# Optimization experiments

Measured on AMD Instinct MI355X. Metric: run time of the kernel, lower is better.

## Reference

```python
import jax, jax.numpy as jnp
import numpy as np

N = 8192
MARGIN = 0.2
LAMB = 0.012
ITERS = 5


def setup_inputs() -> dict:
    key = jax.random.key(0)
    # sims in [0,1): cosine-similarity-like scores; exp(-(1-s)/lamb) needs s near [0,1]
    sims = jax.random.uniform(key, (N, N), dtype=jnp.float32)
    return {"sims": sims}


def _ot(sims):
    # Sinkhorn-Knopp normalization, r = c = ones so (r/u) == 1/u, (c/v) == 1/v
    P = jnp.exp(-(1.0 - sims) / LAMB)
    P = P / jnp.sum(P)  # global normalization (dims [-2,-1])
    for _ in range(ITERS):
        u = P.sum(axis=-1, keepdims=True)   # row sums  [N,1]
        P = P / u
        v = P.sum(axis=-2, keepdims=True)   # col sums  [1,N]
        P = P / v
    return P


def reference(sims):
    P = _ot(sims)
    d = jnp.diagonal(P)                     # [N]
    eye = jnp.eye(P.shape[0], dtype=bool)
    # cost_im: anchor = column diagonal (d[j]); cost_s: anchor = row diagonal (d[i])
    cost_im = jnp.where(eye, 0.0, jnp.maximum(P - d[None, :] + MARGIN, 0.0))
    cost_s = jnp.where(eye, 0.0, jnp.maximum(P - d[:, None] + MARGIN, 0.0))
    # max_violation = False -> sum over all hinge terms
    return cost_s.sum() + cost_im.sum()
```

## Files before the change

### kernel.cpp

```cpp
#include <hip/hip_runtime.h>


#define NN 8192u
#define MARGIN 0.2f
#define KF (1.4426950408889634f / 0.012f)

__device__ __forceinline__ float fexp2(float x) { return __builtin_amdgcn_exp2f(x); }
__device__ __forceinline__ float frcp(float x) { return __builtin_amdgcn_rcpf(x); }

__device__ __forceinline__ void unpk4(uint q, float& f0, float& f1, float& f2,
                                      float& f3) {
  auto lo = __builtin_amdgcn_cvt_pk_f32_fp8((int)q, false);
  auto hi = __builtin_amdgcn_cvt_pk_f32_fp8((int)q, true);
  f0 = lo[0]; f1 = lo[1]; f2 = hi[0]; f3 = hi[1];
}

__device__ __forceinline__ float blk_reduce(float v, float* red) {
#pragma unroll
  for (int off = 32; off; off >>= 1) v += __shfl_down(v, off, 64);
  const int lane = threadIdx.x & 63, wid = threadIdx.x >> 6;
  __syncthreads();
  if (lane == 0) red[wid] = v;
  __syncthreads();
  return red[0] + red[1] + red[2] + red[3];
}

__global__ __launch_bounds__(256) void k_pass0(const float* __restrict__ sims,
                                               uint* __restrict__ Qw,
                                               float* __restrict__ R,
                                               float* __restrict__ Qd,
                                               float* __restrict__ Cs0,
                                               float* __restrict__ out) {
  __shared__ float red[4];
  const uint row = blockIdx.x;
  const uint t = threadIdx.x;
  float acc = 0.f;
#pragma unroll
  for (uint ch = 0; ch < 8; ++ch) {
    const uint col = ch * 1024u + t * 4u;
    const float4 s = *(const float4*)(sims + (size_t)row * NN + col);
    const float p0 = fexp2((s.x - 1.f) * KF);
    const float p1 = fexp2((s.y - 1.f) * KF);
    const float p2 = fexp2((s.z - 1.f) * KF);
    const float p3 = fexp2((s.w - 1.f) * KF);
    int pk = 0;
    pk = __builtin_amdgcn_cvt_pk_fp8_f32(p0, p1, pk, false);
    pk = __builtin_amdgcn_cvt_pk_fp8_f32(p2, p3, pk, true);
    Qw[((size_t)row * NN + col) >> 2] = (uint)pk;
    float q0, q1, q2, q3;
    unpk4((uint)pk, q0, q1, q2, q3);
    acc += (q0 + q1) + (q2 + q3);
    if (col == (row & ~3u)) {
      const uint sel = row & 3u;
      Qd[row] = sel == 0u ? q0 : sel == 1u ? q1 : sel == 2u ? q2 : q3;
    }
  }
  const float s = blk_reduce(acc, red);
  if (t == 0) R[row] = frcp(s);
  if (row < 32u) Cs0[row * 256u + t] = 0.f;
  if (row == 0 && t == 0) *out = 0.f;
}

__global__ __launch_bounds__(256) void k_colmv(const uint* __restrict__ Qw,
                                               const float* __restrict__ R,
                                               float* __restrict__ dst,
                                               float* __restrict__ zero_other) {
  const uint t = threadIdx.x;
  const uint col = blockIdx.x * 1024u + t * 4u;
  const uint row0 = blockIdx.y * 128u;
  if (blockIdx.y == 0u) {
    float4 z; z.x = z.y = z.z = z.w = 0.f;
    *(float4*)(zero_other + col) = z;
  }
  float a0 = 0.f, a1 = 0.f, a2 = 0.f, a3 = 0.f;
  const uint* qp = Qw + (((size_t)row0 * NN + col) >> 2);
#pragma unroll 4
  for (uint rr = 0; rr < 128u; ++rr) {
    const float Rr = R[row0 + rr];
    float f0, f1, f2, f3;
    unpk4(qp[rr * 2048u], f0, f1, f2, f3);
    a0 = fmaf(f0, Rr, a0);
    a1 = fmaf(f1, Rr, a1);
    a2 = fmaf(f2, Rr, a2);
    a3 = fmaf(f3, Rr, a3);
  }
  atomicAdd(dst + col + 0, a0);
  atomicAdd(dst + col + 1, a1);
  atomicAdd(dst + col + 2, a2);
  atomicAdd(dst + col + 3, a3);
}

__global__ __launch_bounds__(256) void k_rowmv(const uint* __restrict__ Qw,
                                               const float* __restrict__ Csrc,
                                               float* __restrict__ R) {
  __shared__ float ldsC[NN];
  __shared__ float red[4];
  const uint t = threadIdx.x;
  for (uint c = t * 4u; c < NN; c += 1024u) {
    const float4 s = *(const float4*)(Csrc + c);
    float4 o;
    o.x = frcp(s.x); o.y = frcp(s.y); o.z = frcp(s.z); o.w = frcp(s.w);
    *(float4*)(ldsC + c) = o;
  }
  __syncthreads();
#pragma unroll
  for (uint r = 0; r < 8u; ++r) {
    const uint row = blockIdx.x * 8u + r;
    float acc = 0.f;
#pragma unroll
    for (uint ch = 0; ch < 2u; ++ch) {
      const uint col = ch * 4096u + t * 16u;
      const float4 c0 = *(const float4*)(ldsC + col);
      const float4 c1 = *(const float4*)(ldsC + col + 4);
      const float4 c2 = *(const float4*)(ldsC + col + 8);
      const float4 c3 = *(const float4*)(ldsC + col + 12);
      const uint4 q = *(const uint4*)(Qw + (size_t)row * 2048u + (col >> 2));
      float a0, a1, a2, a3, b0, b1, b2, b3;
      unpk4(q.x, a0, a1, a2, a3);
      unpk4(q.y, b0, b1, b2, b3);
      acc += a0 * c0.x + a1 * c0.y + a2 * c0.z + a3 * c0.w;
      acc += b0 * c1.x + b1 * c1.y + b2 * c1.z + b3 * c1.w;
      unpk4(q.z, a0, a1, a2, a3);
      unpk4(q.w, b0, b1, b2, b3);
      acc += a0 * c2.x + a1 * c2.y + a2 * c2.z + a3 * c2.w;
      acc += b0 * c3.x + b1 * c3.y + b2 * c3.z + b3 * c3.w;
    }
    const float s = blk_reduce(acc, red);
    if (t == 0) R[row] = frcp(s);
  }
}

__global__ __launch_bounds__(256) void k_loss(const uint* __restrict__ Qw,
                                              const float* __restrict__ R,
                                              const float* __restrict__ Cs,
                                              const float* __restrict__ Qd,
                                              float* __restrict__ out) {
  __shared__ float red[4];
  const uint t = threadIdx.x;
  const uint col = blockIdx.x * 1024u + t * 4u;
  const uint row0 = blockIdx.y * 128u;
  const float4 cs4 = *(const float4*)(Cs + col);
  const float4 r4 = *(const float4*)(R + col);
  const float4 qd4 = *(const float4*)(Qd + col);
  const float ci0 = frcp(cs4.x), ci1 = frcp(cs4.y), ci2 = frcp(cs4.z),
              ci3 = frcp(cs4.w);
  const float d0 = qd4.x * r4.x * ci0;
  const float d1 = qd4.y * r4.y * ci1;
  const float d2 = qd4.z * r4.z * ci2;
  const float d3 = qd4.w * r4.w * ci3;
  float acc = 0.f;
  const uint* qp = Qw + (((size_t)row0 * NN + col) >> 2);
  for (uint rr = 0; rr < 128u; ++rr) {
    const uint row = row0 + rr;
    const float Rr = R[row];
    const float dr = Qd[row] * Rr * frcp(Cs[row]);
    float f0, f1, f2, f3;
    unpk4(qp[rr * 2048u], f0, f1, f2, f3);
    float p, h;
    p = f0 * Rr * ci0;
    h = fmaxf(p - d0 + MARGIN, 0.f) + fmaxf(p - dr + MARGIN, 0.f);
    acc += (row == col + 0u) ? 0.f : h;
    p = f1 * Rr * ci1;
    h = fmaxf(p - d1 + MARGIN, 0.f) + fmaxf(p - dr + MARGIN, 0.f);
    acc += (row == col + 1u) ? 0.f : h;
    p = f2 * Rr * ci2;
    h = fmaxf(p - d2 + MARGIN, 0.f) + fmaxf(p - dr + MARGIN, 0.f);
    acc += (row == col + 2u) ? 0.f : h;
    p = f3 * Rr * ci3;
    h = fmaxf(p - d3 + MARGIN, 0.f) + fmaxf(p - dr + MARGIN, 0.f);
    acc += (row == col + 3u) ? 0.f : h;
  }
  const float s = blk_reduce(acc, red);
  if (t == 0) atomicAdd(out, s);
}

extern "C" void kernel_launch(void* const* d_in, const int* in_sizes, int n_in,
                              void* d_out, int out_size, void* d_ws,
                              size_t ws_size, hipStream_t stream) {
  const float* sims = (const float*)d_in[0];
  float* out = (float*)d_out;
  uint* Qw = (uint*)d_ws;
  float* fb = (float*)((char*)d_ws + (size_t)NN * NN);
  float* R = fb;
  float* Cs[2] = {fb + NN, fb + 2 * NN};
  float* Qd = fb + 3 * NN;

  k_pass0<<<8192, 256, 0, stream>>>(sims, Qw, R, Qd, Cs[0], out);
  for (int k = 0; k < 5; ++k) {
    k_colmv<<<dim3(8, 64), 256, 0, stream>>>(Qw, R, Cs[k & 1], Cs[(k + 1) & 1]);
    if (k < 4) k_rowmv<<<1024, 256, 0, stream>>>(Qw, Cs[k & 1], R);
  }
  k_loss<<<dim3(8, 64), 256, 0, stream>>>(Qw, R, Cs[0], Qd, out);
}
```

Baseline: 563.7 us.

## Fuse all Sinkhorn passes into one persistent kernel with grid barriers

Replaces the sequence of separate exp, column-sum, row-sum and loss kernels with a single persistent kernel of 256 blocks of 1024 threads that synchronize through a global atomic barrier. Each block owns 32 rows, so its row-sum and loss work reuses the same slice of the fp8 matrix. Column sums are built from per-block partials written to a workspace buffer, then reduced and added atomically. This removes launch gaps and changes the cache access pattern. In exchange it depends on all blocks being co-resident and on a ready-flag and counter protocol whose reset across launches may race.

```diff
diff --git a/kernel.cpp b/kernel.cpp
--- a/kernel.cpp
+++ b/kernel.cpp
@@ -4,174 +4,188 @@
 #define NN 8192u
 #define MARGIN 0.2f
 #define KF (1.4426950408889634f / 0.012f)
+#define NBLK 256u
+#define NTHR 1024u
 
 __device__ __forceinline__ float fexp2(float x) { return __builtin_amdgcn_exp2f(x); }
 __device__ __forceinline__ float frcp(float x) { return __builtin_amdgcn_rcpf(x); }
 
-__device__ __forceinline__ void unpk4(uint q, float& f0, float& f1, float& f2,
-                                      float& f3) {
-  auto lo = __builtin_amdgcn_cvt_pk_f32_fp8((int)q, false);
-  auto hi = __builtin_amdgcn_cvt_pk_f32_fp8((int)q, true);
-  f0 = lo[0]; f1 = lo[1]; f2 = hi[0]; f3 = hi[1];
-}
-
-__device__ __forceinline__ float blk_reduce(float v, float* red) {
-#pragma unroll
-  for (int off = 32; off; off >>= 1) v += __shfl_down(v, off, 64);
-  const int lane = threadIdx.x & 63, wid = threadIdx.x >> 6;
+__device__ __forceinline__ void unpk8(uint2 q, float* f) {
+  auto a = __builtin_amdgcn_cvt_pk_f32_fp8((int)q.x, false);
+  auto b = __builtin_amdgcn_cvt_pk_f32_fp8((int)q.x, true);
+  auto c = __builtin_amdgcn_cvt_pk_f32_fp8((int)q.y, false);
+  auto d = __builtin_amdgcn_cvt_pk_f32_fp8((int)q.y, true);
+  f[0] = a[0]; f[1] = a[1]; f[2] = b[0]; f[3] = b[1];
+  f[4] = c[0]; f[5] = c[1]; f[6] = d[0]; f[7] = d[1];
+}
+
+__device__ __forceinline__ void gbarrier(uint* bar, uint n, uint tid) {
   __syncthreads();
-  if (lane == 0) red[wid] = v;
+  if (tid == 0) {
+    __threadfence();
+    atomicAdd(bar, 1u);
+    const uint tgt = NBLK * n;
+    while (atomicAdd(bar, 0u) < tgt) __builtin_amdgcn_s_sleep(8);
+    __threadfence();
+  }
   __syncthreads();
-  return red[0] + red[1] + red[2] + red[3];
-}
-
-__global__ __launch_bounds__(256) void k_pass0(const float* __restrict__ sims,
-                                               uint* __restrict__ Qw,
-                                               float* __restrict__ R,
-                                               float* __restrict__ Qd,
-                                               float* __restrict__ Cs0,
-                                               float* __restrict__ out) {
-  __shared__ float red[4];
-  const uint row = blockIdx.x;
-  const uint t = threadIdx.x;
-  float acc = 0.f;
-#pragma unroll
-  for (uint ch = 0; ch < 8; ++ch) {
-    const uint col = ch * 1024u + t * 4u;
-    const float4 s = *(const float4*)(sims + (size_t)row * NN + col);
-    const float p0 = fexp2((s.x - 1.f) * KF);
-    const float p1 = fexp2((s.y - 1.f) * KF);
-    const float p2 = fexp2((s.z - 1.f) * KF);
-    const float p3 = fexp2((s.w - 1.f) * KF);
-    int pk = 0;
-    pk = __builtin_amdgcn_cvt_pk_fp8_f32(p0, p1, pk, false);
-    pk = __builtin_amdgcn_cvt_pk_fp8_f32(p2, p3, pk, true);
-    Qw[((size_t)row * NN + col) >> 2] = (uint)pk;
-    float q0, q1, q2, q3;
-    unpk4((uint)pk, q0, q1, q2, q3);
-    acc += (q0 + q1) + (q2 + q3);
-    if (col == (row & ~3u)) {
-      const uint sel = row & 3u;
-      Qd[row] = sel == 0u ? q0 : sel == 1u ? q1 : sel == 2u ? q2 : q3;
-    }
-  }
-  const float s = blk_reduce(acc, red);
-  if (t == 0) R[row] = frcp(s);
-  if (row < 32u) Cs0[row * 256u + t] = 0.f;
-  if (row == 0 && t == 0) *out = 0.f;
-}
-
-__global__ __launch_bounds__(256) void k_colmv(const uint* __restrict__ Qw,
-                                               const float* __restrict__ R,
-                                               float* __restrict__ dst,
-                                               float* __restrict__ zero_other) {
-  const uint t = threadIdx.x;
-  const uint col = blockIdx.x * 1024u + t * 4u;
-  const uint row0 = blockIdx.y * 128u;
-  if (blockIdx.y == 0u) {
-    float4 z; z.x = z.y = z.z = z.w = 0.f;
-    *(float4*)(zero_other + col) = z;
-  }
-  float a0 = 0.f, a1 = 0.f, a2 = 0.f, a3 = 0.f;
-  const uint* qp = Qw + (((size_t)row0 * NN + col) >> 2);
-#pragma unroll 4
-  for (uint rr = 0; rr < 128u; ++rr) {
-    const float Rr = R[row0 + rr];
-    float f0, f1, f2, f3;
-    unpk4(qp[rr * 2048u], f0, f1, f2, f3);
-    a0 = fmaf(f0, Rr, a0);
-    a1 = fmaf(f1, Rr, a1);
-    a2 = fmaf(f2, Rr, a2);
-    a3 = fmaf(f3, Rr, a3);
-  }
-  atomicAdd(dst + col + 0, a0);
-  atomicAdd(dst + col + 1, a1);
-  atomicAdd(dst + col + 2, a2);
-  atomicAdd(dst + col + 3, a3);
-}
-
-__global__ __launch_bounds__(256) void k_rowmv(const uint* __restrict__ Qw,
-                                               const float* __restrict__ Csrc,
-                                               float* __restrict__ R) {
-  __shared__ float ldsC[NN];
-  __shared__ float red[4];
-  const uint t = threadIdx.x;
-  for (uint c = t * 4u; c < NN; c += 1024u) {
-    const float4 s = *(const float4*)(Csrc + c);
-    float4 o;
-    o.x = frcp(s.x); o.y = frcp(s.y); o.z = frcp(s.z); o.w = frcp(s.w);
-    *(float4*)(ldsC + c) = o;
+}
+
+__global__ __launch_bounds__(NTHR) void k_fused(
+    const float* __restrict__ sims, uint* __restrict__ Qw,
+    float* __restrict__ part, float* __restrict__ R, float* __restrict__ CsA,
+    float* __restrict__ CsB, float* __restrict__ Qd, uint* __restrict__ ctl,
+    float* __restrict__ out) {
+  const uint b = blockIdx.x, tid = threadIdx.x;
+  const uint w = tid >> 6, lane = tid & 63u;
+  __shared__ float red[512];
+  uint* ready = ctl;
+  uint* bar = ctl + 1;
+
+  if (b == 0 && tid == 0) {
+    atomicExch(bar, 0u);
+    __threadfence();
+    atomicExch(ready, 0xC0FFEEu);
+  }
+  if (b != 0 && tid == 0) {
+    while (atomicAdd(ready, 0u) != 0xC0FFEEu) __builtin_amdgcn_s_sleep(8);
+    __threadfence();
   }
   __syncthreads();
-#pragma unroll
-  for (uint r = 0; r < 8u; ++r) {
-    const uint row = blockIdx.x * 8u + r;
+  uint bn = 0;
+
+#pragma unroll
+  for (uint q = 0; q < 2u; ++q) {
+    const uint row = b * 32u + q * 16u + w;
+    const uint dit = row >> 8, dl = (row >> 2) & 63u, sel = row & 3u;
     float acc = 0.f;
-#pragma unroll
-    for (uint ch = 0; ch < 2u; ++ch) {
-      const uint col = ch * 4096u + t * 16u;
-      const float4 c0 = *(const float4*)(ldsC + col);
-      const float4 c1 = *(const float4*)(ldsC + col + 4);
-      const float4 c2 = *(const float4*)(ldsC + col + 8);
-      const float4 c3 = *(const float4*)(ldsC + col + 12);
-      const uint4 q = *(const uint4*)(Qw + (size_t)row * 2048u + (col >> 2));
-      float a0, a1, a2, a3, b0, b1, b2, b3;
-      unpk4(q.x, a0, a1, a2, a3);
-      unpk4(q.y, b0, b1, b2, b3);
-      acc += a0 * c0.x + a1 * c0.y + a2 * c0.z + a3 * c0.w;
-      acc += b0 * c1.x + b1 * c1.y + b2 * c1.z + b3 * c1.w;
-      unpk4(q.z, a0, a1, a2, a3);
-      unpk4(q.w, b0, b1, b2, b3);
-      acc += a0 * c2.x + a1 * c2.y + a2 * c2.z + a3 * c2.w;
-      acc += b0 * c3.x + b1 * c3.y + b2 * c3.z + b3 * c3.w;
-    }
-    const float s = blk_reduce(acc, red);
-    if (t == 0) R[row] = frcp(s);
-  }
-}
-
-__global__ __launch_bounds__(256) void k_loss(const uint* __restrict__ Qw,
-                                              const float* __restrict__ R,
-                                              const float* __restrict__ Cs,
-                                              const float* __restrict__ Qd,
-                                              float* __restrict__ out) {
-  __shared__ float red[4];
-  const uint t = threadIdx.x;
-  const uint col = blockIdx.x * 1024u + t * 4u;
-  const uint row0 = blockIdx.y * 128u;
-  const float4 cs4 = *(const float4*)(Cs + col);
-  const float4 r4 = *(const float4*)(R + col);
-  const float4 qd4 = *(const float4*)(Qd + col);
-  const float ci0 = frcp(cs4.x), ci1 = frcp(cs4.y), ci2 = frcp(cs4.z),
-              ci3 = frcp(cs4.w);
-  const float d0 = qd4.x * r4.x * ci0;
-  const float d1 = qd4.y * r4.y * ci1;
-  const float d2 = qd4.z * r4.z * ci2;
-  const float d3 = qd4.w * r4.w * ci3;
-  float acc = 0.f;
-  const uint* qp = Qw + (((size_t)row0 * NN + col) >> 2);
-  for (uint rr = 0; rr < 128u; ++rr) {
-    const uint row = row0 + rr;
-    const float Rr = R[row];
-    const float dr = Qd[row] * Rr * frcp(Cs[row]);
-    float f0, f1, f2, f3;
-    unpk4(qp[rr * 2048u], f0, f1, f2, f3);
-    float p, h;
-    p = f0 * Rr * ci0;
-    h = fmaxf(p - d0 + MARGIN, 0.f) + fmaxf(p - dr + MARGIN, 0.f);
-    acc += (row == col + 0u) ? 0.f : h;
-    p = f1 * Rr * ci1;
-    h = fmaxf(p - d1 + MARGIN, 0.f) + fmaxf(p - dr + MARGIN, 0.f);
-    acc += (row == col + 1u) ? 0.f : h;
-    p = f2 * Rr * ci2;
-    h = fmaxf(p - d2 + MARGIN, 0.f) + fmaxf(p - dr + MARGIN, 0.f);
-    acc += (row == col + 2u) ? 0.f : h;
-    p = f3 * Rr * ci3;
-    h = fmaxf(p - d3 + MARGIN, 0.f) + fmaxf(p - dr + MARGIN, 0.f);
-    acc += (row == col + 3u) ? 0.f : h;
-  }
-  const float s = blk_reduce(acc, red);
-  if (t == 0) atomicAdd(out, s);
+    for (uint it = 0; it < 32u; ++it) {
+      const uint col = it * 256u + lane * 4u;
+      const float4 s = *(const float4*)(sims + (size_t)row * NN + col);
+      const float p0 = fexp2((s.x - 1.f) * KF);
+      const float p1 = fexp2((s.y - 1.f) * KF);
+      const float p2 = fexp2((s.z - 1.f) * KF);
+      const float p3 = fexp2((s.w - 1.f) * KF);
+      int pk = 0;
+      pk = __builtin_amdgcn_cvt_pk_fp8_f32(p0, p1, pk, false);
+      pk = __builtin_amdgcn_cvt_pk_fp8_f32(p2, p3, pk, true);
+      Qw[((size_t)row * NN + col) >> 2] = (uint)pk;
+      auto lo = __builtin_amdgcn_cvt_pk_f32_fp8(pk, false);
+      auto hi = __builtin_amdgcn_cvt_pk_f32_fp8(pk, true);
+      acc += (lo[0] + lo[1]) + (hi[0] + hi[1]);
+      if (it == dit && lane == dl)
+        Qd[row] = sel == 0u ? lo[0] : sel == 1u ? lo[1] : sel == 2u ? hi[0] : hi[1];
+    }
+#pragma unroll
+    for (int o = 32; o; o >>= 1) acc += __shfl_down(acc, o, 64);
+    if (lane == 0) R[row] = frcp(acc);
+  }
+  if (tid < 32u) CsA[b * 32u + tid] = 0.f;
+  if (b == 0 && tid == 0) *out = 0.f;
+
+  for (uint k = 0; k < 5u; ++k) {
+    float* dst = (k & 1u) ? CsB : CsA;
+    float* oth = (k & 1u) ? CsA : CsB;
+    gbarrier(bar, ++bn, tid);
+    {
+      const uint j0 = tid * 8u;
+      float a[8];
+#pragma unroll
+      for (int i = 0; i < 8; ++i) a[i] = 0.f;
+      for (uint r = 0; r < 32u; ++r) {
+        const uint row = b * 32u + r;
+        const float Rr = R[row];
+        const uint2 q2 = *(const uint2*)(Qw + (((size_t)row * NN + j0) >> 2));
+        float f[8];
+        unpk8(q2, f);
+#pragma unroll
+        for (int i = 0; i < 8; ++i) a[i] = fmaf(f[i], Rr, a[i]);
+      }
+      *(float4*)(part + (size_t)b * NN + j0) = make_float4(a[0], a[1], a[2], a[3]);
+      *(float4*)(part + (size_t)b * NN + j0 + 4) = make_float4(a[4], a[5], a[6], a[7]);
+    }
+    gbarrier(bar, ++bn, tid);
+    {
+      const uint g = b * NTHR + tid;
+      const uint j = g & (NN - 1u);
+      const uint c = g >> 13;
+      float s = 0.f;
+#pragma unroll
+      for (uint r = 0; r < 8u; ++r) s += part[(size_t)(c * 8u + r) * NN + j];
+      atomicAdd(dst + j, s);
+    }
+    gbarrier(bar, ++bn, tid);
+    if (k < 4u) {
+      const uint j0 = tid * 8u;
+      const float4 c0 = *(const float4*)(dst + j0);
+      const float4 c1 = *(const float4*)(dst + j0 + 4);
+      float cinv[8] = {frcp(c0.x), frcp(c0.y), frcp(c0.z), frcp(c0.w),
+                       frcp(c1.x), frcp(c1.y), frcp(c1.z), frcp(c1.w)};
+      if (tid < 32u) oth[b * 32u + tid] = 0.f;
+      for (uint r = 0; r < 32u; ++r) {
+        const uint row = b * 32u + r;
+        const uint2 q2 = *(const uint2*)(Qw + (((size_t)row * NN + j0) >> 2));
+        float f[8];
+        unpk8(q2, f);
+        float s = f[0] * cinv[0] + f[1] * cinv[1] + f[2] * cinv[2] +
+                  f[3] * cinv[3] + f[4] * cinv[4] + f[5] * cinv[5] +
+                  f[6] * cinv[6] + f[7] * cinv[7];
+#pragma unroll
+        for (int o = 32; o; o >>= 1) s += __shfl_down(s, o, 64);
+        if (lane == 0) red[r * 16u + w] = s;
+      }
+      __syncthreads();
+      if (tid < 32u) {
+        float s = 0.f;
+#pragma unroll
+        for (uint i = 0; i < 16u; ++i) s += red[tid * 16u + i];
+        R[b * 32u + tid] = frcp(s);
+      }
+    }
+  }
+
+  {
+    const uint j0 = tid * 8u;
+    const float4 c0 = *(const float4*)(CsA + j0);
+    const float4 c1 = *(const float4*)(CsA + j0 + 4);
+    const float4 r0 = *(const float4*)(R + j0);
+    const float4 r1 = *(const float4*)(R + j0 + 4);
+    const float4 q0 = *(const float4*)(Qd + j0);
+    const float4 q1 = *(const float4*)(Qd + j0 + 4);
+    float cinv[8] = {frcp(c0.x), frcp(c0.y), frcp(c0.z), frcp(c0.w),
+                     frcp(c1.x), frcp(c1.y), frcp(c1.z), frcp(c1.w)};
+    float dj[8] = {q0.x * r0.x * cinv[0], q0.y * r0.y * cinv[1],
+                   q0.z * r0.z * cinv[2], q0.w * r0.w * cinv[3],
+                   q1.x * r1.x * cinv[4], q1.y * r1.y * cinv[5],
+                   q1.z * r1.z * cinv[6], q1.w * r1.w * cinv[7]};
+    float acc = 0.f;
+    for (uint r = 0; r < 32u; ++r) {
+      const uint row = b * 32u + r;
+      const float Rr = R[row];
+      const float drow = Qd[row] * Rr * frcp(CsA[row]);
+      const uint2 q2 = *(const uint2*)(Qw + (((size_t)row * NN + j0) >> 2));
+      float f[8];
+      unpk8(q2, f);
+#pragma unroll
+      for (uint i = 0; i < 8u; ++i) {
+        const float p = f[i] * Rr * cinv[i];
+        const float h = fmaxf(p - dj[i] + MARGIN, 0.f) +
+                        fmaxf(p - drow + MARGIN, 0.f);
+        acc += (row == j0 + i) ? 0.f : h;
+      }
+    }
+#pragma unroll
+    for (int o = 32; o; o >>= 1) acc += __shfl_down(acc, o, 64);
+    __syncthreads();
+    if (lane == 0) red[w] = acc;
+    __syncthreads();
+    if (tid == 0) {
+      float s = 0.f;
+#pragma unroll
+      for (uint i = 0; i < 16u; ++i) s += red[i];
+      atomicAdd(out, s);
+    }
+  }
 }
 
 extern "C" void kernel_launch(void* const* d_in, const int* in_sizes, int n_in,
@@ -179,16 +193,14 @@
                               size_t ws_size, hipStream_t stream) {
   const float* sims = (const float*)d_in[0];
   float* out = (float*)d_out;
-  uint* Qw = (uint*)d_ws;
-  float* fb = (float*)((char*)d_ws + (size_t)NN * NN);
-  float* R = fb;
-  float* Cs[2] = {fb + NN, fb + 2 * NN};
-  float* Qd = fb + 3 * NN;
-
-  k_pass0<<<8192, 256, 0, stream>>>(sims, Qw, R, Qd, Cs[0], out);
-  for (int k = 0; k < 5; ++k) {
-    k_colmv<<<dim3(8, 64), 256, 0, stream>>>(Qw, R, Cs[k & 1], Cs[(k + 1) & 1]);
-    if (k < 4) k_rowmv<<<1024, 256, 0, stream>>>(Qw, Cs[k & 1], R);
-  }
-  k_loss<<<dim3(8, 64), 256, 0, stream>>>(Qw, R, Cs[0], Qd, out);
-}
+  char* p = (char*)d_ws;
+  uint* Qw = (uint*)p;                       p += (size_t)NN * NN;
+  float* part = (float*)p;                   p += (size_t)NBLK * NN * 4;
+  float* R = (float*)p;                      p += NN * 4;
+  float* CsA = (float*)p;                    p += NN * 4;
+  float* CsB = (float*)p;                    p += NN * 4;
+  float* Qd = (float*)p;                     p += NN * 4;
+  uint* ctl = (uint*)p;
+
+  k_fused<<<NBLK, NTHR, 0, stream>>>(sims, Qw, part, R, CsA, CsB, Qd, ctl, out);
+}
```

Result: slower. 875.9 us (+55.4%).
